# Kernel optimization log

Measured on AMD Instinct MI355X. Metric: run time of the kernel, lower is better.

## Reference

```python
import jax, jax.numpy as jnp
import numpy as np

N = 16384      # nodes
E = 262144     # edges (avg degree 16)
F_IN = 128     # n_feat
D = 128        # n_dims
C = 10         # n_clss
SIGMA = 1.0    # args.sigma


def setup_inputs() -> dict:
    key = jax.random.key(0)
    ks = jax.random.split(key, 12)
    s_in = 1.0 / np.sqrt(F_IN)
    s_d = 1.0 / np.sqrt(D)
    s_c = 1.0 / np.sqrt(2 * D)
    return {
        "x": jax.random.normal(ks[0], (N, F_IN), jnp.float32),
        "edge_index": jax.random.randint(ks[1], (2, E), 0, N, dtype=jnp.int32),
        # SAGEConv1: lin_l (neighbors, with bias) and lin_r (root, no bias)
        "W1l": jax.random.normal(ks[2], (D, F_IN), jnp.float32) * s_in,
        "b1l": jnp.zeros((D,), jnp.float32),
        "W1r": jax.random.normal(ks[3], (D, F_IN), jnp.float32) * s_in,
        # SAGEConv2
        "W2l": jax.random.normal(ks[4], (D, D), jnp.float32) * s_d,
        "b2l": jnp.zeros((D,), jnp.float32),
        "W2r": jax.random.normal(ks[5], (D, D), jnp.float32) * s_d,
        # anchor vector (init.uniform_ -> U[0,1))
        "aux": jax.random.uniform(ks[6], (D,), jnp.float32),
        # classifier on [h, z] concat
        "Wc": jax.random.normal(ks[7], (C, 2 * D), jnp.float32) * s_c,
        "bc": jnp.zeros((C,), jnp.float32),
    }


def _sage_conv(x, src, dst, Wl, bl, Wr):
    # PyG SAGEConv (mean aggr): out = lin_l(mean_{j in N(i)} x_j) + lin_r(x_i)
    msg = x[src]                                                  # [E, d]
    agg = jax.ops.segment_sum(msg, dst, num_segments=N)           # [N, d]
    deg = jax.ops.segment_sum(jnp.ones((src.shape[0],), x.dtype), dst,
                              num_segments=N)                     # [N]
    agg = agg / jnp.maximum(deg, 1.0)[:, None]
    return agg @ Wl.T + bl + x @ Wr.T


def _kernel_aggregate(h, aux, sigma):
    # cosine similarity to anchor (torch eps = 1e-8)
    eps = 1e-8
    hn = jnp.maximum(jnp.linalg.norm(h, axis=-1), eps)            # [N]
    an = jnp.maximum(jnp.linalg.norm(aux), eps)
    score = (h @ aux) / (hn * an)                                 # [N]
    diff = score[None, :] - score[:, None]                        # [N, N]
    kappa = jnp.exp(-(diff * diff) / (sigma * sigma))             # [N, N]
    return (kappa @ h) / jnp.sum(kappa, axis=1, keepdims=True)    # [N, d]


def reference(x, W1l, b1l, W1r, W2l, b2l, W2r, aux, Wc, bc, edge_index):
    src, dst = edge_index[0], edge_index[1]
    h = jax.nn.relu(_sage_conv(x, src, dst, W1l, b1l, W1r))
    # dropout is identity at inference
    h = _sage_conv(h, src, dst, W2l, b2l, W2r)
    z = _kernel_aggregate(h, aux, SIGMA)
    return jnp.concatenate([h, z], axis=-1) @ Wc.T + bc           # [N, C]
```

## Files before the change

kernel.cpp:

```cpp
#include <hip/hip_runtime.h>
#include <hip/hip_bf16.h>

#define D 128
#define KTERMS 16

typedef __attribute__((ext_vector_type(8))) short bf16x8;
typedef __attribute__((ext_vector_type(4))) float f32x4;

__device__ inline short rne_bf16(float f) {
    union { float f; unsigned u; } v; v.f = f;
    unsigned r = (v.u + 0x7fffu + ((v.u >> 16) & 1u)) >> 16;
    return (short)r;
}
__device__ inline float bf16_to_f(unsigned s) {
    union { unsigned u; float f; } v; v.u = s << 16;
    return v.f;
}
__device__ inline unsigned pk2(float a, float b) {
    return (unsigned)(unsigned short)rne_bf16(a) | ((unsigned)(unsigned short)rne_bf16(b) << 16);
}
__device__ inline void addv(float* acc, uint4 v) {
    acc[0] += bf16_to_f(v.x & 0xffffu);
    acc[1] += bf16_to_f(v.x >> 16);
    acc[2] += bf16_to_f(v.y & 0xffffu);
    acc[3] += bf16_to_f(v.y >> 16);
    acc[4] += bf16_to_f(v.z & 0xffffu);
    acc[5] += bf16_to_f(v.z >> 16);
    acc[6] += bf16_to_f(v.w & 0xffffu);
    acc[7] += bf16_to_f(v.w >> 16);
}

__global__ __launch_bounds__(256) void prep_kernel(const float* __restrict__ x,
                                                   short* __restrict__ xb,
                                                   const float* __restrict__ W1l,
                                                   const float* __restrict__ W1r,
                                                   const float* __restrict__ W2l,
                                                   const float* __restrict__ W2r,
                                                   short* __restrict__ Bc1,
                                                   short* __restrict__ Bc2,
                                                   int* __restrict__ zero_ints,
                                                   float* __restrict__ zero_f) {
    int b = blockIdx.x;
    int tid = threadIdx.x;
    if (b < 1024) {
        int base = (b * 256 + tid) * 8;
        const float4 a = *reinterpret_cast<const float4*>(&x[base]);
        const float4 c = *reinterpret_cast<const float4*>(&x[base + 4]);
        uint4 o;
        o.x = pk2(a.x, a.y);
        o.y = pk2(a.z, a.w);
        o.z = pk2(c.x, c.y);
        o.w = pk2(c.z, c.w);
        *reinterpret_cast<uint4*>(&xb[base]) = o;
    } else if (b < 1280) {
        int idx = (b - 1024) * 256 + tid;
        int layer = idx >> 15;
        int rem = idx & 32767;
        int c = rem >> 8, k = rem & 255;
        const float* Wl = layer ? W2l : W1l;
        const float* Wr = layer ? W2r : W1r;
        float v = (k < 128) ? Wl[c * 128 + k] : Wr[c * 128 + (k - 128)];
        short* Bc = layer ? Bc2 : Bc1;
        Bc[c * 256 + k] = rne_bf16(v);
    } else if (b < 1312) {
        int idx = (b - 1280) * 256 + tid;
        reinterpret_cast<int4*>(zero_ints)[idx] = make_int4(0, 0, 0, 0);
    } else {
        for (int e = tid; e < KTERMS * D + KTERMS; e += 256) zero_f[e] = 0.0f;
    }
}

__global__ __launch_bounds__(256) void degi_kernel(const int* __restrict__ dst,
                                                   int* __restrict__ degi, int E) {
    int e = blockIdx.x * 256 + threadIdx.x;
    if (e < E) atomicAdd(&degi[dst[e]], 1);
}

__global__ __launch_bounds__(1024) void scan_kernel(const int* __restrict__ degi,
                                                    int* __restrict__ rowptr,
                                                    float* __restrict__ invdeg, int N) {
    __shared__ int part[1024];
    int tid = threadIdx.x;
    int base = tid * 16;
    int loc[16];
    int s = 0;
#pragma unroll
    for (int i = 0; i < 16; i++) {
        int d = degi[base + i];
        loc[i] = s; s += d;
        invdeg[base + i] = 1.0f / fmaxf((float)d, 1.0f);
    }
    part[tid] = s;
    __syncthreads();
    for (int off = 1; off < 1024; off <<= 1) {
        int t = (tid >= off) ? part[tid - off] : 0;
        __syncthreads();
        if (tid >= off) part[tid] += t;
        __syncthreads();
    }
    int prefix = part[tid] - s;
#pragma unroll
    for (int i = 0; i < 16; i++) rowptr[base + i] = prefix + loc[i];
    if (tid == 1023) rowptr[N] = prefix + s;
}

__global__ __launch_bounds__(256) void fill_kernel(const int* __restrict__ src,
                                                   const int* __restrict__ dst,
                                                   const int* __restrict__ rowptr,
                                                   int* __restrict__ cursor,
                                                   int* __restrict__ csr_src, int E) {
    int e = blockIdx.x * 256 + threadIdx.x;
    if (e < E) {
        int d = dst[e];
        int pos = atomicAdd(&cursor[d], 1);
        csr_src[rowptr[d] + pos] = src[e];
    }
}

__global__ __launch_bounds__(256) void sage_fused_kernel(const short* __restrict__ Asrc,
                                                         const short* __restrict__ Bc,
                                                         const float* __restrict__ bias,
                                                         const int* __restrict__ rowptr,
                                                         const int* __restrict__ csr_src,
                                                         const float* __restrict__ invdeg,
                                                         const float* __restrict__ aux,
                                                         short* __restrict__ outb,
                                                         float* __restrict__ outf,
                                                         float* __restrict__ sbuf,
                                                         float* __restrict__ wbuf,
                                                         int relu, int score) {
    __shared__ short aggl[16 * 128];
    __shared__ float sdot[16][4];
    __shared__ float snrm[16][4];
    __shared__ float an_s;

    int lane = threadIdx.x & 63;
    int wid = threadIdx.x >> 6;
    int row0 = blockIdx.x * 16;
    int sub = lane >> 4, sl = lane & 15;

    if (score && wid == 0) {
        float2 av = *reinterpret_cast<const float2*>(&aux[lane * 2]);
        float na = av.x * av.x + av.y * av.y;
        for (int m = 1; m < 64; m <<= 1) na += __shfl_xor(na, m);
        if (lane == 0) an_s = fmaxf(sqrtf(na), 1e-8f);
    }

    int r = wid * 4 + sub;
    int node = row0 + r;
    int beg = rowptr[node], end = rowptr[node + 1];
    float acc8[8] = {0.0f, 0.0f, 0.0f, 0.0f, 0.0f, 0.0f, 0.0f, 0.0f};
    int j = beg;
    for (; j + 3 < end; j += 4) {
        int s0 = csr_src[j], s1 = csr_src[j + 1], s2 = csr_src[j + 2], s3 = csr_src[j + 3];
        uint4 v0 = *reinterpret_cast<const uint4*>(&Asrc[(size_t)s0 * D + sl * 8]);
        uint4 v1 = *reinterpret_cast<const uint4*>(&Asrc[(size_t)s1 * D + sl * 8]);
        uint4 v2 = *reinterpret_cast<const uint4*>(&Asrc[(size_t)s2 * D + sl * 8]);
        uint4 v3 = *reinterpret_cast<const uint4*>(&Asrc[(size_t)s3 * D + sl * 8]);
        addv(acc8, v0); addv(acc8, v1); addv(acc8, v2); addv(acc8, v3);
    }
    for (; j < end; j++) {
        int s = csr_src[j];
        uint4 v = *reinterpret_cast<const uint4*>(&Asrc[(size_t)s * D + sl * 8]);
        addv(acc8, v);
    }
    float inv = invdeg[node];
    uint4 o;
    o.x = pk2(acc8[0] * inv, acc8[1] * inv);
    o.y = pk2(acc8[2] * inv, acc8[3] * inv);
    o.z = pk2(acc8[4] * inv, acc8[5] * inv);
    o.w = pk2(acc8[6] * inv, acc8[7] * inv);
    int wbyte = (r * 256 + sl * 16) ^ ((r & 7) << 4);
    *reinterpret_cast<uint4*>(reinterpret_cast<char*>(aggl) + wbyte) = o;
    __syncthreads();

    int colbase = wid * 32;
    int rl = lane & 15;
    int kg = lane >> 4;
    int koff = kg * 8;
    int arow_g = row0 + rl;

    f32x4 acc[2];
    acc[0] = (f32x4){0.0f, 0.0f, 0.0f, 0.0f};
    acc[1] = (f32x4){0.0f, 0.0f, 0.0f, 0.0f};

#pragma unroll
    for (int kc = 0; kc < 8; kc++) {
        bf16x8 a;
        if (kc < 4) {
            int rbyte = (rl * 256 + kc * 64 + kg * 16) ^ ((rl & 7) << 4);
            a = *reinterpret_cast<const bf16x8*>(reinterpret_cast<const char*>(aggl) + rbyte);
        } else {
            int k = (kc - 4) * 32 + koff;
            a = *reinterpret_cast<const bf16x8*>(&Asrc[(size_t)arow_g * D + k]);
        }
#pragma unroll
        for (int t = 0; t < 2; t++) {
            int col = colbase + t * 16 + rl;
            bf16x8 b = *reinterpret_cast<const bf16x8*>(&Bc[(size_t)col * 256 + kc * 32 + koff]);
            acc[t] = __builtin_amdgcn_mfma_f32_16x16x32_bf16(a, b, acc[t], 0, 0, 0);
        }
    }

    int rbase = kg * 4;
    float dotp[4] = {0.0f, 0.0f, 0.0f, 0.0f};
    float nrmp[4] = {0.0f, 0.0f, 0.0f, 0.0f};
#pragma unroll
    for (int t = 0; t < 2; t++) {
        int col = colbase + t * 16 + rl;
        float bv = bias[col];
        float av = score ? aux[col] : 0.0f;
#pragma unroll
        for (int rr = 0; rr < 4; rr++) {
            float v = acc[t][rr] + bv;
            if (relu) v = fmaxf(v, 0.0f);
            int grow = row0 + rbase + rr;
            if (outf) outf[(size_t)grow * D + col] = v;
            else outb[(size_t)grow * D + col] = rne_bf16(v);
            dotp[rr] += v * av;
            nrmp[rr] += v * v;
        }
    }

    if (score) {
#pragma unroll
        for (int m = 1; m < 16; m <<= 1) {
#pragma unroll
            for (int rr = 0; rr < 4; rr++) {
                dotp[rr] += __shfl_xor(dotp[rr], m);
                nrmp[rr] += __shfl_xor(nrmp[rr], m);
            }
        }
        if (rl == 0) {
#pragma unroll
            for (int rr = 0; rr < 4; rr++) {
                sdot[rbase + rr][wid] = dotp[rr];
                snrm[rbase + rr][wid] = nrmp[rr];
            }
        }
        __syncthreads();
        int tid = threadIdx.x;
        if (tid < 16) {
            float dot = sdot[tid][0] + sdot[tid][1] + sdot[tid][2] + sdot[tid][3];
            float nh  = snrm[tid][0] + snrm[tid][1] + snrm[tid][2] + snrm[tid][3];
            float hn = fmaxf(sqrtf(nh), 1e-8f);
            float sc = dot / (hn * an_s);
            sbuf[row0 + tid] = sc;
            wbuf[row0 + tid] = expf(-sc * sc);
        }
    }
}

__global__ __launch_bounds__(512) void moments_kernel(const float* __restrict__ h,
                                                      const float* __restrict__ sbuf,
                                                      const float* __restrict__ wbuf,
                                                      float* __restrict__ M,
                                                      float* __restrict__ mden, int N) {
    __shared__ float lds[8 * KTERMS * D];
    __shared__ float ldsm[8 * KTERMS];
    int tid = threadIdx.x;
    int w = tid >> 6, lane = tid & 63;
    int j0 = blockIdx.x * 64 + w * 8;

    float2 acc[KTERMS];
    float macc[KTERMS];
#pragma unroll
    for (int k = 0; k < KTERMS; k++) { acc[k] = make_float2(0.0f, 0.0f); macc[k] = 0.0f; }

    for (int j = j0; j < j0 + 8; j++) {
        float sj = sbuf[j];
        float wj = wbuf[j];
        float2 hv = *reinterpret_cast<const float2*>(&h[(size_t)j * D + lane * 2]);
        float coef = wj;
#pragma unroll
        for (int k = 0; k < KTERMS; k++) {
            acc[k].x += coef * hv.x;
            acc[k].y += coef * hv.y;
            macc[k] += coef;
            coef *= sj;
        }
    }

#pragma unroll
    for (int k = 0; k < KTERMS; k++) {
        lds[(w * KTERMS + k) * D + lane * 2]     = acc[k].x;
        lds[(w * KTERMS + k) * D + lane * 2 + 1] = acc[k].y;
    }
    if (lane == 0) {
#pragma unroll
        for (int k = 0; k < KTERMS; k++) ldsm[w * KTERMS + k] = macc[k];
    }
    __syncthreads();

    for (int e = tid; e < KTERMS * D; e += 512) {
        float s = 0.0f;
#pragma unroll
        for (int ww = 0; ww < 8; ww++) s += lds[ww * KTERMS * D + e];
        atomicAdd(&M[e], s);
    }
    if (tid < KTERMS) {
        float s = 0.0f;
#pragma unroll
        for (int ww = 0; ww < 8; ww++) s += ldsm[ww * KTERMS + tid];
        atomicAdd(&mden[tid], s);
    }
}

__global__ __launch_bounds__(128) void zcls_kernel(const float* __restrict__ M,
                                                   const float* __restrict__ mden,
                                                   const float* __restrict__ sbuf,
                                                   const float* __restrict__ h,
                                                   const float* __restrict__ Wc,
                                                   const float* __restrict__ bc,
                                                   float* __restrict__ out, int N) {
    const float A[KTERMS] = {1.0f, 2.0f, 2.0f, 1.3333334f, 0.6666667f, 0.26666668f,
                             0.08888889f, 0.025396826f, 0.0063492064f, 0.0014109347f,
                             2.8218695e-4f, 5.1306718e-5f, 8.5511196e-6f, 1.3155569e-6f,
                             1.8793670e-7f, 2.5058226e-8f};
    __shared__ float Ml[KTERMS * D];
    __shared__ float ml[KTERMS];
    __shared__ float wls[10 * 256];
    __shared__ float red[10][2];
    int tid = threadIdx.x;
    int lane = tid & 63, w = tid >> 6;
#pragma unroll
    for (int k = 0; k < KTERMS; k++) Ml[k * D + tid] = M[k * D + tid];
    if (tid < KTERMS) ml[tid] = mden[tid];
    for (int e = tid; e < 10 * 256; e += 128) wls[e] = Wc[e];
    __syncthreads();

    int n0 = blockIdx.x * 16;
    for (int n = n0; n < n0 + 16; n++) {
        float si = sbuf[n];
        float num = 0.0f, den = 0.0f, p = 1.0f;
#pragma unroll
        for (int k = 0; k < KTERMS; k++) {
            float ck = A[k] * p;
            num += ck * Ml[k * D + tid];
            den += ck * ml[k];
            p *= si;
        }
        float zc = num / den;
        float hc = h[(size_t)n * D + tid];

        float part[10];
#pragma unroll
        for (int c = 0; c < 10; c++)
            part[c] = hc * wls[c * 256 + tid] + zc * wls[c * 256 + 128 + tid];
#pragma unroll
        for (int m = 1; m < 64; m <<= 1) {
#pragma unroll
            for (int c = 0; c < 10; c++) part[c] += __shfl_xor(part[c], m);
        }
        if (lane == 0) {
#pragma unroll
            for (int c = 0; c < 10; c++) red[c][w] = part[c];
        }
        __syncthreads();
        if (tid < 10) out[(size_t)n * 10 + tid] = red[tid][0] + red[tid][1] + bc[tid];
        __syncthreads();
    }
}

extern "C" void kernel_launch(void* const* d_in, const int* in_sizes, int n_in,
                              void* d_out, int out_size, void* d_ws, size_t ws_size,
                              hipStream_t stream) {
    const float* x   = (const float*)d_in[0];
    const int*   ei  = (const int*)d_in[1];
    const float* W1l = (const float*)d_in[2];
    const float* b1l = (const float*)d_in[3];
    const float* W1r = (const float*)d_in[4];
    const float* W2l = (const float*)d_in[5];
    const float* b2l = (const float*)d_in[6];
    const float* W2r = (const float*)d_in[7];
    const float* aux = (const float*)d_in[8];
    const float* Wc  = (const float*)d_in[9];
    const float* bc  = (const float*)d_in[10];
    float* out = (float*)d_out;

    const int N = in_sizes[0] / D;
    const int E = in_sizes[1] / 2;
    const int* srcArr = ei;
    const int* dstArr = ei + E;
    const size_t ND = (size_t)N * D;

    int* ip = (int*)d_ws;
    int* degi    = ip; ip += N;
    int* cursor  = ip; ip += N;
    int* rowptr  = ip; ip += N + 1;
    int* csr_src = ip; ip += E;
    uintptr_t up = ((uintptr_t)ip + 15) & ~(uintptr_t)15;
    short* sp = (short*)up;
    short* xb   = sp; sp += ND;
    short* h1b  = sp; sp += ND;
    short* Bc1  = sp; sp += 128 * 256;
    short* Bc2  = sp; sp += 128 * 256;
    up = ((uintptr_t)sp + 15) & ~(uintptr_t)15;
    float* p = (float*)up;
    float* invdeg = p; p += N;
    float* sbuf   = p; p += N;
    float* wbuf   = p; p += N;
    float* M      = p; p += KTERMS * D;
    float* mden   = p; p += KTERMS;
    float* h2     = p; p += ND;

    prep_kernel<<<1313, 256, 0, stream>>>(x, xb, W1l, W1r, W2l, W2r, Bc1, Bc2, degi, M);

    degi_kernel<<<(E + 255) / 256, 256, 0, stream>>>(dstArr, degi, E);
    scan_kernel<<<1, 1024, 0, stream>>>(degi, rowptr, invdeg, N);
    fill_kernel<<<(E + 255) / 256, 256, 0, stream>>>(srcArr, dstArr, rowptr, cursor, csr_src, E);

    sage_fused_kernel<<<N / 16, 256, 0, stream>>>(xb, Bc1, b1l, rowptr, csr_src, invdeg,
                                                  aux, h1b, nullptr, nullptr, nullptr, 1, 0);
    sage_fused_kernel<<<N / 16, 256, 0, stream>>>(h1b, Bc2, b2l, rowptr, csr_src, invdeg,
                                                  aux, nullptr, h2, sbuf, wbuf, 0, 1);

    moments_kernel<<<N / 64, 512, 0, stream>>>(h2, sbuf, wbuf, M, mden, N);

    zcls_kernel<<<N / 16, 128, 0, stream>>>(M, mden, sbuf, h2, Wc, bc, out, N);
}
```

Before: 134.1 us.

## Fuse moment accumulation into second SAGE layer with sharded atomics

```diff
diff --git a/kernel.cpp b/kernel.cpp
--- a/kernel.cpp
+++ b/kernel.cpp
@@ -3,6 +3,7 @@
 
 #define D 128
 #define KTERMS 16
+#define NSHARD 16
 
 typedef __attribute__((ext_vector_type(8))) short bf16x8;
 typedef __attribute__((ext_vector_type(4))) float f32x4;
@@ -66,7 +67,9 @@
         int idx = (b - 1280) * 256 + tid;
         reinterpret_cast<int4*>(zero_ints)[idx] = make_int4(0, 0, 0, 0);
     } else {
-        for (int e = tid; e < KTERMS * D + KTERMS; e += 256) zero_f[e] = 0.0f;
+        int idx = (b - 1312) * 256 + tid;
+        if (idx < (NSHARD * (KTERMS * D + KTERMS)) / 4)
+            reinterpret_cast<float4*>(zero_f)[idx] = make_float4(0.f, 0.f, 0.f, 0.f);
     }
 }
 
@@ -127,11 +130,14 @@
                                                          short* __restrict__ outb,
                                                          float* __restrict__ outf,
                                                          float* __restrict__ sbuf,
-                                                         float* __restrict__ wbuf,
+                                                         float* __restrict__ Msh,
+                                                         float* __restrict__ msh,
                                                          int relu, int score) {
     __shared__ short aggl[16 * 128];
     __shared__ float sdot[16][4];
     __shared__ float snrm[16][4];
+    __shared__ float sws[16];
+    __shared__ float wws[16];
     __shared__ float an_s;
 
     int lane = threadIdx.x & 63;
@@ -149,8 +155,23 @@
     int r = wid * 4 + sub;
     int node = row0 + r;
     int beg = rowptr[node], end = rowptr[node + 1];
+    float inv = invdeg[node];
     float acc8[8] = {0.0f, 0.0f, 0.0f, 0.0f, 0.0f, 0.0f, 0.0f, 0.0f};
     int j = beg;
+    for (; j + 7 < end; j += 8) {
+        int s0 = csr_src[j], s1 = csr_src[j + 1], s2 = csr_src[j + 2], s3 = csr_src[j + 3];
+        int s4 = csr_src[j + 4], s5 = csr_src[j + 5], s6 = csr_src[j + 6], s7 = csr_src[j + 7];
+        uint4 v0 = *reinterpret_cast<const uint4*>(&Asrc[(size_t)s0 * D + sl * 8]);
+        uint4 v1 = *reinterpret_cast<const uint4*>(&Asrc[(size_t)s1 * D + sl * 8]);
+        uint4 v2 = *reinterpret_cast<const uint4*>(&Asrc[(size_t)s2 * D + sl * 8]);
+        uint4 v3 = *reinterpret_cast<const uint4*>(&Asrc[(size_t)s3 * D + sl * 8]);
+        uint4 v4 = *reinterpret_cast<const uint4*>(&Asrc[(size_t)s4 * D + sl * 8]);
+        uint4 v5 = *reinterpret_cast<const uint4*>(&Asrc[(size_t)s5 * D + sl * 8]);
+        uint4 v6 = *reinterpret_cast<const uint4*>(&Asrc[(size_t)s6 * D + sl * 8]);
+        uint4 v7 = *reinterpret_cast<const uint4*>(&Asrc[(size_t)s7 * D + sl * 8]);
+        addv(acc8, v0); addv(acc8, v1); addv(acc8, v2); addv(acc8, v3);
+        addv(acc8, v4); addv(acc8, v5); addv(acc8, v6); addv(acc8, v7);
+    }
     for (; j + 3 < end; j += 4) {
         int s0 = csr_src[j], s1 = csr_src[j + 1], s2 = csr_src[j + 2], s3 = csr_src[j + 3];
         uint4 v0 = *reinterpret_cast<const uint4*>(&Asrc[(size_t)s0 * D + sl * 8]);
@@ -164,7 +185,6 @@
         uint4 v = *reinterpret_cast<const uint4*>(&Asrc[(size_t)s * D + sl * 8]);
         addv(acc8, v);
     }
-    float inv = invdeg[node];
     uint4 o;
     o.x = pk2(acc8[0] * inv, acc8[1] * inv);
     o.y = pk2(acc8[2] * inv, acc8[3] * inv);
@@ -203,22 +223,31 @@
     }
 
     int rbase = kg * 4;
+    float vkeep0[4], vkeep1[4];
     float dotp[4] = {0.0f, 0.0f, 0.0f, 0.0f};
     float nrmp[4] = {0.0f, 0.0f, 0.0f, 0.0f};
-#pragma unroll
-    for (int t = 0; t < 2; t++) {
-        int col = colbase + t * 16 + rl;
-        float bv = bias[col];
-        float av = score ? aux[col] : 0.0f;
+    {
+        int col0 = colbase + rl;
+        int col1 = colbase + 16 + rl;
+        float bv0 = bias[col0], bv1 = bias[col1];
+        float av0 = score ? aux[col0] : 0.0f;
+        float av1 = score ? aux[col1] : 0.0f;
 #pragma unroll
         for (int rr = 0; rr < 4; rr++) {
-            float v = acc[t][rr] + bv;
-            if (relu) v = fmaxf(v, 0.0f);
+            float v0 = acc[0][rr] + bv0;
+            float v1 = acc[1][rr] + bv1;
+            if (relu) { v0 = fmaxf(v0, 0.0f); v1 = fmaxf(v1, 0.0f); }
             int grow = row0 + rbase + rr;
-            if (outf) outf[(size_t)grow * D + col] = v;
-            else outb[(size_t)grow * D + col] = rne_bf16(v);
-            dotp[rr] += v * av;
-            nrmp[rr] += v * v;
+            if (outf) {
+                outf[(size_t)grow * D + col0] = v0;
+                outf[(size_t)grow * D + col1] = v1;
+            } else {
+                outb[(size_t)grow * D + col0] = rne_bf16(v0);
+                outb[(size_t)grow * D + col1] = rne_bf16(v1);
+            }
+            vkeep0[rr] = v0; vkeep1[rr] = v1;
+            dotp[rr] += v0 * av0 + v1 * av1;
+            nrmp[rr] += v0 * v0 + v1 * v1;
         }
     }
 
@@ -240,74 +269,68 @@
         }
         __syncthreads();
         int tid = threadIdx.x;
+        int shard = blockIdx.x & (NSHARD - 1);
         if (tid < 16) {
             float dot = sdot[tid][0] + sdot[tid][1] + sdot[tid][2] + sdot[tid][3];
             float nh  = snrm[tid][0] + snrm[tid][1] + snrm[tid][2] + snrm[tid][3];
             float hn = fmaxf(sqrtf(nh), 1e-8f);
             float sc = dot / (hn * an_s);
+            float w = expf(-sc * sc);
             sbuf[row0 + tid] = sc;
-            wbuf[row0 + tid] = expf(-sc * sc);
-        }
-    }
-}
-
-__global__ __launch_bounds__(512) void moments_kernel(const float* __restrict__ h,
-                                                      const float* __restrict__ sbuf,
-                                                      const float* __restrict__ wbuf,
-                                                      float* __restrict__ M,
-                                                      float* __restrict__ mden, int N) {
-    __shared__ float lds[8 * KTERMS * D];
-    __shared__ float ldsm[8 * KTERMS];
-    int tid = threadIdx.x;
-    int w = tid >> 6, lane = tid & 63;
-    int j0 = blockIdx.x * 64 + w * 8;
-
-    float2 acc[KTERMS];
-    float macc[KTERMS];
-#pragma unroll
-    for (int k = 0; k < KTERMS; k++) { acc[k] = make_float2(0.0f, 0.0f); macc[k] = 0.0f; }
-
-    for (int j = j0; j < j0 + 8; j++) {
-        float sj = sbuf[j];
-        float wj = wbuf[j];
-        float2 hv = *reinterpret_cast<const float2*>(&h[(size_t)j * D + lane * 2]);
-        float coef = wj;
-#pragma unroll
-        for (int k = 0; k < KTERMS; k++) {
-            acc[k].x += coef * hv.x;
-            acc[k].y += coef * hv.y;
-            macc[k] += coef;
-            coef *= sj;
-        }
-    }
-
-#pragma unroll
-    for (int k = 0; k < KTERMS; k++) {
-        lds[(w * KTERMS + k) * D + lane * 2]     = acc[k].x;
-        lds[(w * KTERMS + k) * D + lane * 2 + 1] = acc[k].y;
-    }
-    if (lane == 0) {
-#pragma unroll
-        for (int k = 0; k < KTERMS; k++) ldsm[w * KTERMS + k] = macc[k];
-    }
-    __syncthreads();
-
-    for (int e = tid; e < KTERMS * D; e += 512) {
-        float s = 0.0f;
-#pragma unroll
-        for (int ww = 0; ww < 8; ww++) s += lds[ww * KTERMS * D + e];
-        atomicAdd(&M[e], s);
-    }
-    if (tid < KTERMS) {
-        float s = 0.0f;
-#pragma unroll
-        for (int ww = 0; ww < 8; ww++) s += ldsm[ww * KTERMS + tid];
-        atomicAdd(&mden[tid], s);
-    }
-}
-
-__global__ __launch_bounds__(128) void zcls_kernel(const float* __restrict__ M,
-                                                   const float* __restrict__ mden,
+            sws[tid] = sc;
+            wws[tid] = w;
+            float* ms = msh + shard * KTERMS;
+            float coef = w;
+#pragma unroll
+            for (int k = 0; k < KTERMS; k++) {
+                float v = coef;
+#pragma unroll
+                for (int m = 1; m < 16; m <<= 1) v += __shfl_xor(v, m);
+                if (tid == 0) atomicAdd(&ms[k], v);
+                coef *= sc;
+            }
+        }
+        __syncthreads();
+
+        float c0[KTERMS], c1[KTERMS];
+#pragma unroll
+        for (int k = 0; k < KTERMS; k++) { c0[k] = 0.0f; c1[k] = 0.0f; }
+#pragma unroll
+        for (int rr = 0; rr < 4; rr++) {
+            int row = rbase + rr;
+            float srow = sws[row];
+            float coef = wws[row];
+            float v0 = vkeep0[rr], v1 = vkeep1[rr];
+#pragma unroll
+            for (int k = 0; k < KTERMS; k++) {
+                c0[k] += coef * v0;
+                c1[k] += coef * v1;
+                coef *= srow;
+            }
+        }
+#pragma unroll
+        for (int m = 16; m < 64; m <<= 1) {
+#pragma unroll
+            for (int k = 0; k < KTERMS; k++) {
+                c0[k] += __shfl_xor(c0[k], m);
+                c1[k] += __shfl_xor(c1[k], m);
+            }
+        }
+        if (kg == 0) {
+            float* Ms = Msh + shard * (KTERMS * D);
+            int col0 = colbase + rl;
+            int col1 = colbase + 16 + rl;
+#pragma unroll
+            for (int k = 0; k < KTERMS; k++) {
+                atomicAdd(&Ms[k * D + col0], c0[k]);
+                atomicAdd(&Ms[k * D + col1], c1[k]);
+            }
+        }
+    }
+}
+
+__global__ __launch_bounds__(128) void zcls_kernel(const float* __restrict__ Msh,
+                                                   const float* __restrict__ msh,
                                                    const float* __restrict__ sbuf,
                                                    const float* __restrict__ h,
                                                    const float* __restrict__ Wc,
@@ -324,8 +347,18 @@
     int tid = threadIdx.x;
     int lane = tid & 63, w = tid >> 6;
 #pragma unroll
-    for (int k = 0; k < KTERMS; k++) Ml[k * D + tid] = M[k * D + tid];
-    if (tid < KTERMS) ml[tid] = mden[tid];
+    for (int k = 0; k < KTERMS; k++) {
+        float s = 0.0f;
+#pragma unroll
+        for (int sh = 0; sh < NSHARD; sh++) s += Msh[sh * (KTERMS * D) + k * D + tid];
+        Ml[k * D + tid] = s;
+    }
+    if (tid < KTERMS) {
+        float s = 0.0f;
+#pragma unroll
+        for (int sh = 0; sh < NSHARD; sh++) s += msh[sh * KTERMS + tid];
+        ml[tid] = s;
+    }
     for (int e = tid; e < 10 * 256; e += 128) wls[e] = Wc[e];
     __syncthreads();
 
@@ -399,23 +432,20 @@
     float* p = (float*)up;
     float* invdeg = p; p += N;
     float* sbuf   = p; p += N;
-    float* wbuf   = p; p += N;
-    float* M      = p; p += KTERMS * D;
-    float* mden   = p; p += KTERMS;
+    float* Msh    = p; p += NSHARD * KTERMS * D;
+    float* msh    = p; p += NSHARD * KTERMS;
     float* h2     = p; p += ND;
 
-    prep_kernel<<<1313, 256, 0, stream>>>(x, xb, W1l, W1r, W2l, W2r, Bc1, Bc2, degi, M);
+    prep_kernel<<<1345, 256, 0, stream>>>(x, xb, W1l, W1r, W2l, W2r, Bc1, Bc2, degi, Msh);
 
     degi_kernel<<<(E + 255) / 256, 256, 0, stream>>>(dstArr, degi, E);
     scan_kernel<<<1, 1024, 0, stream>>>(degi, rowptr, invdeg, N);
     fill_kernel<<<(E + 255) / 256, 256, 0, stream>>>(srcArr, dstArr, rowptr, cursor, csr_src, E);
 
     sage_fused_kernel<<<N / 16, 256, 0, stream>>>(xb, Bc1, b1l, rowptr, csr_src, invdeg,
-                                                  aux, h1b, nullptr, nullptr, nullptr, 1, 0);
+                                                  aux, h1b, nullptr, nullptr, nullptr, nullptr, 1, 0);
     sage_fused_kernel<<<N / 16, 256, 0, stream>>>(h1b, Bc2, b2l, rowptr, csr_src, invdeg,
-                                                  aux, nullptr, h2, sbuf, wbuf, 0, 1);
-
-    moments_kernel<<<N / 64, 512, 0, stream>>>(h2, sbuf, wbuf, M, mden, N);
-
-    zcls_kernel<<<N / 16, 128, 0, stream>>>(M, mden, sbuf, h2, Wc, bc, out, N);
-}
+                                                  aux, nullptr, h2, sbuf, Msh, msh, 0, 1);
+
+    zcls_kernel<<<N / 16, 128, 0, stream>>>(Msh, msh, sbuf, h2, Wc, bc, out, N);
+}
```

Result: slower. 155.1 us (+15.7%).
